# Kernel tuning notes

Hardware: AMD Instinct MI355X
Metric: run time of the kernel (lower is better)

## Reference

```python
import jax, jax.numpy as jnp
import numpy as np

B, T, V, E, H, C = 256, 512, 100000, 128, 256, 2


def setup_inputs() -> dict:
    key = jax.random.key(0)
    ks = jax.random.split(key, 14)
    lens = jax.random.randint(ks[0], (B,), 1, T + 1)          # valid lengths in [1, T]
    seqs = jax.random.randint(ks[1], (B, T), 1, V)            # tokens 1..V-1 (0 = pad)
    valid = jnp.arange(T)[None, :] < lens[:, None]
    seqs = jnp.where(valid, seqs, 0)                           # padding_idx = 0
    embed = jax.random.normal(ks[2], (V, E), dtype=jnp.float32) * 0.02
    embed = embed.at[0].set(0.0)                               # padding row zeroed (torch padding_idx)
    s = 1.0 / np.sqrt(H)
    u = lambda k, sh: jax.random.uniform(k, sh, minval=-s, maxval=s, dtype=jnp.float32)
    return {
        "seqs": seqs, "lens": lens, "embed": embed,
        "W_ih_f": u(ks[3], (3 * H, E)), "W_hh_f": u(ks[4], (3 * H, H)),
        "b_ih_f": u(ks[5], (3 * H,)),   "b_hh_f": u(ks[6], (3 * H,)),
        "W_ih_b": u(ks[7], (3 * H, E)), "W_hh_b": u(ks[8], (3 * H, H)),
        "b_ih_b": u(ks[9], (3 * H,)),   "b_hh_b": u(ks[10], (3 * H,)),
        "W_fc": u(ks[11], (C, 2 * H)),  "b_fc": u(ks[12], (C,)),
    }


def _gru_last_hidden(x, W_ih, W_hh, b_ih, b_hh, lens):
    """Run a single-direction GRU over x [B,T,E]; return hidden at step lens-1, [B,H].
    PyTorch GRU gate order: r, z, n."""
    xp = jnp.einsum('bte,ge->btg', x, W_ih) + b_ih             # [B,T,3H], one big GEMM up front

    def step(h, xp_t):                                          # xp_t: [B,3H]
        hp = h @ W_hh.T + b_hh
        r = jax.nn.sigmoid(xp_t[:, :H] + hp[:, :H])
        z = jax.nn.sigmoid(xp_t[:, H:2 * H] + hp[:, H:2 * H])
        n = jnp.tanh(xp_t[:, 2 * H:] + r * hp[:, 2 * H:])
        h_new = (1.0 - z) * n + z * h
        return h_new, h_new

    h0 = jnp.zeros((x.shape[0], H), dtype=x.dtype)
    _, hs = jax.lax.scan(step, h0, jnp.swapaxes(xp, 0, 1))     # hs: [T,B,H]
    return hs[lens - 1, jnp.arange(x.shape[0])]                # hidden at last valid step


def reference(seqs, lens, embed, W_ih_f, W_hh_f, b_ih_f, b_hh_f,
              W_ih_b, W_hh_b, b_ih_b, b_hh_b, W_fc, b_fc):
    x = embed[seqs]                                            # [B,T,E]
    # forward direction: final hidden at t = len-1 (packed-sequence semantics)
    h_f = _gru_last_hidden(x, W_ih_f, W_hh_f, b_ih_f, b_hh_f, lens)
    # backward direction: reverse each sequence within its valid length, then same scan
    idx = jnp.clip(lens[:, None] - 1 - jnp.arange(T)[None, :], 0, T - 1)  # [B,T]
    x_rev = jnp.take_along_axis(x, idx[:, :, None], axis=1)
    h_b = _gru_last_hidden(x_rev, W_ih_b, W_hh_b, b_ih_b, b_hh_b, lens)
    h = jnp.concatenate([h_f, h_b], axis=1)                    # [B,2H]
    return h @ W_fc.T + b_fc                                   # [B,C]
```

## Files before the change

kernel.cpp:

```cpp
#include <hip/hip_runtime.h>
#include <cstdint>
#include <cstddef>

#define B_   256
#define T_   512
#define E_   128
#define H_   256

typedef _Float16 f16x8 __attribute__((ext_vector_type(8)));
typedef _Float16 f16x4 __attribute__((ext_vector_type(4)));
typedef float    f32x4 __attribute__((ext_vector_type(4)));

__device__ __forceinline__ float sigm(float x) {
  return __builtin_amdgcn_rcpf(1.f + __expf(-x));
}
__device__ __forceinline__ float tanh_(float x) {
  float e = __expf(2.f * x);
  return 1.f - 2.f * __builtin_amdgcn_rcpf(1.f + e);
}
__device__ __forceinline__ void poll_ge(const int* p, int v) {
  while (__hip_atomic_load(p, __ATOMIC_ACQUIRE, __HIP_MEMORY_SCOPE_AGENT) < v)
    __builtin_amdgcn_s_sleep(4);
}

__global__ __launch_bounds__(256) void prep_kernel(
    const float* __restrict__ whhf, const float* __restrict__ whhb,
    const float* __restrict__ wihf, const float* __restrict__ wihb,
    _Float16* __restrict__ WSW,
    const int* __restrict__ lens, int* __restrict__ order, int* __restrict__ flags)
{
  if (blockIdx.x == 288) {
    int i = threadIdx.x;
    for (int k = i; k < 1024; k += 256) flags[k] = 0;
    for (int k = i; k < 512;  k += 256) flags[1024 + k] = -1;
    int li = lens[i];
    int rank = 0;
    for (int k = 0; k < B_; ++k) {
      int lk = lens[k];
      rank += (lk > li) || (lk == li && k < i);
    }
    order[rank] = i;
    return;
  }
  int idx = blockIdx.x * 256 + threadIdx.x;
  int lane = idx & 63;
  int tile = (idx >> 6) % 48;
  int kc   = (idx / 3072) % 12;
  int dir  = idx / 36864;
  int ncol = tile * 16 + (lane & 15);
  int quad = lane >> 4;
  const float* src;
  if (kc < 8) {
    const float* w = dir ? whhb : whhf;
    src = w + (size_t)ncol * H_ + kc * 32 + quad * 8;
  } else {
    const float* w = dir ? wihb : wihf;
    src = w + (size_t)ncol * E_ + (kc - 8) * 32 + quad * 8;
  }
  f16x8 v;
  #pragma unroll
  for (int j = 0; j < 8; ++j) v[j] = (_Float16)src[j];
  *(f16x8*)(WSW + (size_t)idx * 8) = v;
}

#define XPSLAB 196608
__global__ __launch_bounds__(512, 1) void fused_kernel(
    const _Float16* __restrict__ WSW, const int* __restrict__ seqs,
    const float* __restrict__ embed,
    const float* __restrict__ bihf, const float* __restrict__ bhhf,
    const float* __restrict__ bihb, const float* __restrict__ bhhb,
    const int* __restrict__ lens, const int* __restrict__ order,
    _Float16* __restrict__ XP, int* __restrict__ FLAGS, float* __restrict__ hcat)
{
  __shared__ __align__(16) char smem[147968];
  __shared__ int s_row[16], s_len[16];

  const int bid = blockIdx.x, tid = threadIdx.x;
  const int w = tid >> 6, lane = tid & 63, lm = lane & 15, lq = lane >> 4;

  if (bid < 32) {
    const int g = bid, dir = g & 1, grp = g >> 1;
    _Float16* wl = (_Float16*)smem;
    _Float16* hb = (_Float16*)(smem + 131072);
    if (tid < 16) { int r = order[grp * 16 + tid]; s_row[tid] = r; s_len[tid] = lens[r]; }
    for (int i = tid; i < 2 * 16 * 264; i += 512) hb[i] = (_Float16)0.f;

    const _Float16* wsd = WSW + (size_t)dir * 294912 + (size_t)lane * 8;
    #pragma unroll
    for (int kc = 0; kc < 8; ++kc) {
      *(f16x8*)(wl + ((w * 2 + 0) * 8 + kc) * 512 + lane * 8) =
          *(const f16x8*)(wsd + (size_t)kc * 24576 + (32 + 2 * w) * 512);
      *(f16x8*)(wl + ((w * 2 + 1) * 8 + kc) * 512 + lane * 8) =
          *(const f16x8*)(wsd + (size_t)kc * 24576 + (33 + 2 * w) * 512);
    }
    f16x8 wh[4][8];
    #pragma unroll
    for (int kc = 0; kc < 8; ++kc) {
      wh[0][kc] = *(const f16x8*)(wsd + (size_t)kc * 24576 + (2 * w)      * 512);
      wh[1][kc] = *(const f16x8*)(wsd + (size_t)kc * 24576 + (2 * w + 1)  * 512);
      wh[2][kc] = *(const f16x8*)(wsd + (size_t)kc * 24576 + (16 + 2 * w) * 512);
      wh[3][kc] = *(const f16x8*)(wsd + (size_t)kc * 24576 + (17 + 2 * w) * 512);
    }
    #pragma unroll
    for (int s = 0; s < 4; ++s)
      #pragma unroll
      for (int kc = 0; kc < 8; ++kc)
        asm volatile("" : "+a"(wh[s][kc]));
    const float* bhh = dir ? bhhb : bhhf;
    f16x4 bhn[2];
    #pragma unroll
    for (int th = 0; th < 2; ++th) {
      float4 b = *(const float4*)(bhh + 512 + 32 * w + th * 16 + lq * 4);
      bhn[th][0] = (_Float16)b.x; bhn[th][1] = (_Float16)b.y;
      bhn[th][2] = (_Float16)b.z; bhn[th][3] = (_Float16)b.w;
    }
    __syncthreads();
    const int len_l = s_len[lm];
    int ml = 1;
    #pragma unroll
    for (int i = 0; i < 16; ++i) ml = max(ml, s_len[i]);

    int* doneP  = FLAGS + 1024 + g * 16;
    const int* readyA = FLAGS + g * 32;
    const int* readyB = FLAGS + g * 32 + 16;
    float h32r[2][4] = {};

    for (int t = 0; t < ml; ++t) {
      if ((t & 15) == 0) {
        if (tid == 0) {
          if (t) __hip_atomic_store(doneP, (t >> 4) - 1,
                                    __ATOMIC_RELEASE, __HIP_MEMORY_SCOPE_AGENT);
          poll_ge(readyA, (t >> 4) + 1);
          poll_ge(readyB, (t >> 4) + 1);
        }
        __syncthreads();
      }
      const _Float16* sb = XP + ((size_t)((((t >> 4) & 1) * 32 + g)) * 16 + (t & 15)) * 12288
                           + lq * 64 + lm * 4;
      f16x4 xp[6];
      xp[0] = *(const f16x4*)(sb + (2 * w)      * 256);
      xp[1] = *(const f16x4*)(sb + (2 * w + 1)  * 256);
      xp[2] = *(const f16x4*)(sb + (16 + 2 * w) * 256);
      xp[3] = *(const f16x4*)(sb + (17 + 2 * w) * 256);
      xp[4] = *(const f16x4*)(sb + (32 + 2 * w) * 256);
      xp[5] = *(const f16x4*)(sb + (33 + 2 * w) * 256);

      f32x4 acc[6] = {};
      #pragma unroll
      for (int i = 0; i < 4; ++i) {
        acc[4][i] = (float)bhn[0][i];
        acc[5][i] = (float)bhn[1][i];
      }
      const _Float16* hrow = hb + ((size_t)(t & 1) * 16 + lm) * 264 + lq * 8;
      #pragma unroll
      for (int kc = 0; kc < 8; ++kc) {
        f16x8 hf = *(const f16x8*)(hrow + kc * 32);
        acc[0] = __builtin_amdgcn_mfma_f32_16x16x32_f16(wh[0][kc], hf, acc[0], 0, 0, 0);
        acc[1] = __builtin_amdgcn_mfma_f32_16x16x32_f16(wh[1][kc], hf, acc[1], 0, 0, 0);
        acc[2] = __builtin_amdgcn_mfma_f32_16x16x32_f16(wh[2][kc], hf, acc[2], 0, 0, 0);
        acc[3] = __builtin_amdgcn_mfma_f32_16x16x32_f16(wh[3][kc], hf, acc[3], 0, 0, 0);
        f16x8 w4 = *(const f16x8*)(wl + ((w * 2 + 0) * 8 + kc) * 512 + lane * 8);
        acc[4] = __builtin_amdgcn_mfma_f32_16x16x32_f16(w4, hf, acc[4], 0, 0, 0);
        f16x8 w5 = *(const f16x8*)(wl + ((w * 2 + 1) * 8 + kc) * 512 + lane * 8);
        acc[5] = __builtin_amdgcn_mfma_f32_16x16x32_f16(w5, hf, acc[5], 0, 0, 0);
      }
      #pragma unroll
      for (int th = 0; th < 2; ++th) {
        f16x4 pk;
        #pragma unroll
        for (int i = 0; i < 4; ++i) {
          float r = sigm((float)xp[th][i]     + acc[th][i]);
          float z = sigm((float)xp[2 + th][i] + acc[2 + th][i]);
          float n = tanh_((float)xp[4 + th][i] + r * acc[4 + th][i]);
          float hn = (t < len_l) ? (n + z * (h32r[th][i] - n)) : h32r[th][i];
          h32r[th][i] = hn;
          pk[i] = (_Float16)hn;
        }
        *(f16x4*)(hb + ((size_t)((t + 1) & 1) * 16 + lm) * 264 + 32 * w + th * 16 + lq * 4) = pk;
      }
      __syncthreads();
    }
    if (tid == 0)
      __hip_atomic_store(doneP, 999, __ATOMIC_RELEASE, __HIP_MEMORY_SCOPE_AGENT);
    {
      const int rowb = s_row[lm];
      #pragma unroll
      for (int th = 0; th < 2; ++th) {
        float4 o; o.x = h32r[th][0]; o.y = h32r[th][1]; o.z = h32r[th][2]; o.w = h32r[th][3];
        *(float4*)(&hcat[(size_t)rowb * (2 * H_) + dir * H_ + 32 * w + th * 16 + lq * 4]) = o;
      }
    }
  } else {
    const int k_ = bid - 32;
    const int g = (k_ & 7) + 8 * (k_ >> 4), half = (k_ >> 3) & 1;
    const int dir = g & 1, grp = g >> 1;
    _Float16* xs = (_Float16*)smem;
    if (tid < 16) { int r = order[grp * 16 + tid]; s_row[tid] = r; s_len[tid] = lens[r]; }
    __syncthreads();
    int ml = 1;
    #pragma unroll
    for (int i = 0; i < 16; ++i) ml = max(ml, s_len[i]);
    const int nch = (ml + 15) >> 4;

    const int chain = tid >> 5, q = tid & 31;
    const int rowb = s_row[chain], lenr = s_len[chain];
    const _Float16* wsd = WSW + (size_t)dir * 294912 + (size_t)lane * 8;
    const float* bih = dir ? bihb : bihf;
    const float* bhh = dir ? bhhb : bhhf;
    const int* doneP = FLAGS + 1024 + g * 16;
    int* readyP = FLAGS + g * 32 + half * 16;

    f16x8 wA[6][4];
    float bb[6][4];
    #pragma unroll
    for (int ti = 0; ti < 6; ++ti) {
      const int tile = w + 8 * ti;
      #pragma unroll
      for (int kc = 0; kc < 4; ++kc)
        wA[ti][kc] = *(const f16x8*)(wsd + (size_t)(8 + kc) * 24576 + tile * 512);
      float4 bias = *(const float4*)(bih + tile * 16 + lq * 4);
      if (tile < 32) {
        float4 b2 = *(const float4*)(bhh + tile * 16 + lq * 4);
        bias.x += b2.x; bias.y += b2.y; bias.z += b2.z; bias.w += b2.w;
      }
      bb[ti][0] = bias.x; bb[ti][1] = bias.y; bb[ti][2] = bias.z; bb[ti][3] = bias.w;
    }

    for (int c = 0; c < nch; ++c) {
      if (c >= 2) { if (tid == 0) poll_ge(doneP, c - 2); __syncthreads(); }
      _Float16* slab = XP + (size_t)((c & 1) * 32 + g) * XPSLAB;
      #pragma unroll
      for (int batch = 0; batch < 2; ++batch) {
        #pragma unroll
        for (int sb = 0; sb < 4; ++sb) {
          int s = c * 16 + half * 8 + batch * 4 + sb;
          int p = dir ? (lenr - 1 - s) : s;
          p = min(max(p, 0), T_ - 1);
          int tok = seqs[(size_t)rowb * T_ + p];
          float4 f = *(const float4*)(embed + (size_t)tok * E_ + q * 4);
          f16x4 h4; h4[0] = (_Float16)f.x; h4[1] = (_Float16)f.y;
          h4[2] = (_Float16)f.z; h4[3] = (_Float16)f.w;
          *(f16x4*)(xs + ((size_t)sb * 16 + chain) * 136 + q * 4) = h4;
        }
        __syncthreads();
        f16x8 bx[4][4];
        #pragma unroll
        for (int sb = 0; sb < 4; ++sb)
          #pragma unroll
          for (int kc = 0; kc < 4; ++kc)
            bx[sb][kc] = *(const f16x8*)(xs + ((size_t)sb * 16 + lm) * 136 + kc * 32 + lq * 8);
        #pragma unroll
        for (int ti = 0; ti < 6; ++ti) {
          const int tile = w + 8 * ti;
          f32x4 acc[4] = {};
          #pragma unroll
          for (int kc = 0; kc < 4; ++kc) {
            acc[0] = __builtin_amdgcn_mfma_f32_16x16x32_f16(wA[ti][kc], bx[0][kc], acc[0], 0, 0, 0);
            acc[1] = __builtin_amdgcn_mfma_f32_16x16x32_f16(wA[ti][kc], bx[1][kc], acc[1], 0, 0, 0);
            acc[2] = __builtin_amdgcn_mfma_f32_16x16x32_f16(wA[ti][kc], bx[2][kc], acc[2], 0, 0, 0);
            acc[3] = __builtin_amdgcn_mfma_f32_16x16x32_f16(wA[ti][kc], bx[3][kc], acc[3], 0, 0, 0);
          }
          #pragma unroll
          for (int sb = 0; sb < 4; ++sb) {
            int s_local = half * 8 + batch * 4 + sb;
            f16x4 o;
            #pragma unroll
            for (int i = 0; i < 4; ++i) o[i] = (_Float16)(acc[sb][i] + bb[ti][i]);
            *(f16x4*)(slab + (size_t)s_local * 12288 + tile * 256 + lq * 64 + lm * 4) = o;
          }
        }
        __syncthreads();
      }
      if (tid == 0)
        __hip_atomic_store(readyP, c + 1, __ATOMIC_RELEASE, __HIP_MEMORY_SCOPE_AGENT);
    }
  }
}

__global__ __launch_bounds__(512) void fc_kernel(
    const float* __restrict__ hcat, const float* __restrict__ wfc,
    const float* __restrict__ bfc, float* __restrict__ out)
{
  const int b = blockIdx.x, t = threadIdx.x;
  float h  = hcat[(size_t)b * 512 + t];
  float p0 = h * wfc[t];
  float p1 = h * wfc[512 + t];
  #pragma unroll
  for (int off = 32; off > 0; off >>= 1) {
    p0 += __shfl_down(p0, off);
    p1 += __shfl_down(p1, off);
  }
  __shared__ float s0[8], s1[8];
  if ((t & 63) == 0) { s0[t >> 6] = p0; s1[t >> 6] = p1; }
  __syncthreads();
  if (t == 0) {
    float a = bfc[0], c = bfc[1];
    #pragma unroll
    for (int i = 0; i < 8; ++i) { a += s0[i]; c += s1[i]; }
    out[b * 2 + 0] = a;
    out[b * 2 + 1] = c;
  }
}

extern "C" void kernel_launch(void* const* d_in, const int* in_sizes, int n_in,
                              void* d_out, int out_size, void* d_ws, size_t ws_size,
                              hipStream_t stream)
{
  (void)in_sizes; (void)n_in; (void)out_size; (void)ws_size;
  const int*   seqs  = (const int*)d_in[0];
  const int*   lens  = (const int*)d_in[1];
  const float* embed = (const float*)d_in[2];
  const float* wihf  = (const float*)d_in[3];
  const float* whhf  = (const float*)d_in[4];
  const float* bihf  = (const float*)d_in[5];
  const float* bhhf  = (const float*)d_in[6];
  const float* wihb  = (const float*)d_in[7];
  const float* whhb  = (const float*)d_in[8];
  const float* bihb  = (const float*)d_in[9];
  const float* bhhb  = (const float*)d_in[10];
  const float* wfc   = (const float*)d_in[11];
  const float* bfc   = (const float*)d_in[12];
  float* out = (float*)d_out;

  char* ws = (char*)d_ws;
  _Float16* WSW = (_Float16*)ws;
  size_t off = 1179648;
  _Float16* XP  = (_Float16*)(ws + off); off += (size_t)2 * 32 * XPSLAB * 2;
  float* HCAT   = (float*)(ws + off);    off += (size_t)B_ * 2 * H_ * 4;
  int* ORDER    = (int*)(ws + off);      off += 1024;
  int* FLAGS    = (int*)(ws + off);      off += 6144;

  prep_kernel<<<289, 256, 0, stream>>>(whhf, whhb, wihf, wihb, WSW, lens, ORDER, FLAGS);
  fused_kernel<<<96, 512, 0, stream>>>(WSW, seqs, embed, bihf, bhhf, bihb, bhhb,
                                       lens, ORDER, XP, FLAGS, HCAT);
  fc_kernel<<<B_, 512, 0, stream>>>(HCAT, wfc, bfc, out);
}
```

Measured before the change: 1.161 ms.

## Halve fused kernel block to 256 threads, doubling per-wave GRU gate tiles

```diff
diff --git a/kernel.cpp b/kernel.cpp
--- a/kernel.cpp
+++ b/kernel.cpp
@@ -64,7 +64,7 @@
 }
 
 #define XPSLAB 196608
-__global__ __launch_bounds__(512, 1) void fused_kernel(
+__global__ __launch_bounds__(256, 1) void fused_kernel(
     const _Float16* __restrict__ WSW, const int* __restrict__ seqs,
     const float* __restrict__ embed,
     const float* __restrict__ bihf, const float* __restrict__ bhhf,
@@ -83,34 +83,36 @@
     _Float16* wl = (_Float16*)smem;
     _Float16* hb = (_Float16*)(smem + 131072);
     if (tid < 16) { int r = order[grp * 16 + tid]; s_row[tid] = r; s_len[tid] = lens[r]; }
-    for (int i = tid; i < 2 * 16 * 264; i += 512) hb[i] = (_Float16)0.f;
+    for (int i = tid; i < 2 * 16 * 264; i += 256) hb[i] = (_Float16)0.f;
 
     const _Float16* wsd = WSW + (size_t)dir * 294912 + (size_t)lane * 8;
     #pragma unroll
-    for (int kc = 0; kc < 8; ++kc) {
-      *(f16x8*)(wl + ((w * 2 + 0) * 8 + kc) * 512 + lane * 8) =
-          *(const f16x8*)(wsd + (size_t)kc * 24576 + (32 + 2 * w) * 512);
-      *(f16x8*)(wl + ((w * 2 + 1) * 8 + kc) * 512 + lane * 8) =
-          *(const f16x8*)(wsd + (size_t)kc * 24576 + (33 + 2 * w) * 512);
-    }
-    f16x8 wh[4][8];
-    #pragma unroll
-    for (int kc = 0; kc < 8; ++kc) {
-      wh[0][kc] = *(const f16x8*)(wsd + (size_t)kc * 24576 + (2 * w)      * 512);
-      wh[1][kc] = *(const f16x8*)(wsd + (size_t)kc * 24576 + (2 * w + 1)  * 512);
-      wh[2][kc] = *(const f16x8*)(wsd + (size_t)kc * 24576 + (16 + 2 * w) * 512);
-      wh[3][kc] = *(const f16x8*)(wsd + (size_t)kc * 24576 + (17 + 2 * w) * 512);
-    }
-    #pragma unroll
-    for (int s = 0; s < 4; ++s)
+    for (int th = 0; th < 4; ++th)
       #pragma unroll
       for (int kc = 0; kc < 8; ++kc)
-        asm volatile("" : "+a"(wh[s][kc]));
+        *(f16x8*)(wl + (((w * 4 + th) * 8) + kc) * 512 + lane * 8) =
+            *(const f16x8*)(wsd + (size_t)kc * 24576 + (32 + 4 * w + th) * 512);
+
+    f16x8 whr[4][8], whz[4][8];
+    #pragma unroll
+    for (int th = 0; th < 4; ++th)
+      #pragma unroll
+      for (int kc = 0; kc < 8; ++kc) {
+        whr[th][kc] = *(const f16x8*)(wsd + (size_t)kc * 24576 + (4 * w + th)      * 512);
+        whz[th][kc] = *(const f16x8*)(wsd + (size_t)kc * 24576 + (16 + 4 * w + th) * 512);
+      }
+    #pragma unroll
+    for (int th = 0; th < 4; ++th)
+      #pragma unroll
+      for (int kc = 0; kc < 8; ++kc) {
+        asm volatile("" : "+a"(whr[th][kc]));
+        asm volatile("" : "+a"(whz[th][kc]));
+      }
     const float* bhh = dir ? bhhb : bhhf;
-    f16x4 bhn[2];
-    #pragma unroll
-    for (int th = 0; th < 2; ++th) {
-      float4 b = *(const float4*)(bhh + 512 + 32 * w + th * 16 + lq * 4);
+    f16x4 bhn[4];
+    #pragma unroll
+    for (int th = 0; th < 4; ++th) {
+      float4 b = *(const float4*)(bhh + 512 + 64 * w + th * 16 + lq * 4);
       bhn[th][0] = (_Float16)b.x; bhn[th][1] = (_Float16)b.y;
       bhn[th][2] = (_Float16)b.z; bhn[th][3] = (_Float16)b.w;
     }
@@ -123,7 +125,7 @@
     int* doneP  = FLAGS + 1024 + g * 16;
     const int* readyA = FLAGS + g * 32;
     const int* readyB = FLAGS + g * 32 + 16;
-    float h32r[2][4] = {};
+    float h32r[4][4] = {};
 
     for (int t = 0; t < ml; ++t) {
       if ((t & 15) == 0) {
@@ -137,46 +139,45 @@
       }
       const _Float16* sb = XP + ((size_t)((((t >> 4) & 1) * 32 + g)) * 16 + (t & 15)) * 12288
                            + lq * 64 + lm * 4;
-      f16x4 xp[6];
-      xp[0] = *(const f16x4*)(sb + (2 * w)      * 256);
-      xp[1] = *(const f16x4*)(sb + (2 * w + 1)  * 256);
-      xp[2] = *(const f16x4*)(sb + (16 + 2 * w) * 256);
-      xp[3] = *(const f16x4*)(sb + (17 + 2 * w) * 256);
-      xp[4] = *(const f16x4*)(sb + (32 + 2 * w) * 256);
-      xp[5] = *(const f16x4*)(sb + (33 + 2 * w) * 256);
-
-      f32x4 acc[6] = {};
-      #pragma unroll
-      for (int i = 0; i < 4; ++i) {
-        acc[4][i] = (float)bhn[0][i];
-        acc[5][i] = (float)bhn[1][i];
-      }
+      f16x4 xr[4], xz[4], xn[4];
+      #pragma unroll
+      for (int th = 0; th < 4; ++th) {
+        xr[th] = *(const f16x4*)(sb + (4 * w + th)      * 256);
+        xz[th] = *(const f16x4*)(sb + (16 + 4 * w + th) * 256);
+        xn[th] = *(const f16x4*)(sb + (32 + 4 * w + th) * 256);
+      }
+
+      f32x4 accr[4] = {}, accz[4] = {}, accn[4];
+      #pragma unroll
+      for (int th = 0; th < 4; ++th)
+        #pragma unroll
+        for (int i = 0; i < 4; ++i) accn[th][i] = (float)bhn[th][i];
+
       const _Float16* hrow = hb + ((size_t)(t & 1) * 16 + lm) * 264 + lq * 8;
       #pragma unroll
       for (int kc = 0; kc < 8; ++kc) {
         f16x8 hf = *(const f16x8*)(hrow + kc * 32);
-        acc[0] = __builtin_amdgcn_mfma_f32_16x16x32_f16(wh[0][kc], hf, acc[0], 0, 0, 0);
-        acc[1] = __builtin_amdgcn_mfma_f32_16x16x32_f16(wh[1][kc], hf, acc[1], 0, 0, 0);
-        acc[2] = __builtin_amdgcn_mfma_f32_16x16x32_f16(wh[2][kc], hf, acc[2], 0, 0, 0);
-        acc[3] = __builtin_amdgcn_mfma_f32_16x16x32_f16(wh[3][kc], hf, acc[3], 0, 0, 0);
-        f16x8 w4 = *(const f16x8*)(wl + ((w * 2 + 0) * 8 + kc) * 512 + lane * 8);
-        acc[4] = __builtin_amdgcn_mfma_f32_16x16x32_f16(w4, hf, acc[4], 0, 0, 0);
-        f16x8 w5 = *(const f16x8*)(wl + ((w * 2 + 1) * 8 + kc) * 512 + lane * 8);
-        acc[5] = __builtin_amdgcn_mfma_f32_16x16x32_f16(w5, hf, acc[5], 0, 0, 0);
-      }
-      #pragma unroll
-      for (int th = 0; th < 2; ++th) {
+        #pragma unroll
+        for (int th = 0; th < 4; ++th) {
+          f16x8 wn = *(const f16x8*)(wl + (((w * 4 + th) * 8) + kc) * 512 + lane * 8);
+          accr[th] = __builtin_amdgcn_mfma_f32_16x16x32_f16(whr[th][kc], hf, accr[th], 0, 0, 0);
+          accz[th] = __builtin_amdgcn_mfma_f32_16x16x32_f16(whz[th][kc], hf, accz[th], 0, 0, 0);
+          accn[th] = __builtin_amdgcn_mfma_f32_16x16x32_f16(wn,          hf, accn[th], 0, 0, 0);
+        }
+      }
+      #pragma unroll
+      for (int th = 0; th < 4; ++th) {
         f16x4 pk;
         #pragma unroll
         for (int i = 0; i < 4; ++i) {
-          float r = sigm((float)xp[th][i]     + acc[th][i]);
-          float z = sigm((float)xp[2 + th][i] + acc[2 + th][i]);
-          float n = tanh_((float)xp[4 + th][i] + r * acc[4 + th][i]);
+          float r = sigm((float)xr[th][i] + accr[th][i]);
+          float z = sigm((float)xz[th][i] + accz[th][i]);
+          float n = tanh_((float)xn[th][i] + r * accn[th][i]);
           float hn = (t < len_l) ? (n + z * (h32r[th][i] - n)) : h32r[th][i];
           h32r[th][i] = hn;
           pk[i] = (_Float16)hn;
         }
-        *(f16x4*)(hb + ((size_t)((t + 1) & 1) * 16 + lm) * 264 + 32 * w + th * 16 + lq * 4) = pk;
+        *(f16x4*)(hb + ((size_t)((t + 1) & 1) * 16 + lm) * 264 + 64 * w + th * 16 + lq * 4) = pk;
       }
       __syncthreads();
     }
@@ -185,9 +186,9 @@
     {
       const int rowb = s_row[lm];
       #pragma unroll
-      for (int th = 0; th < 2; ++th) {
+      for (int th = 0; th < 4; ++th) {
         float4 o; o.x = h32r[th][0]; o.y = h32r[th][1]; o.z = h32r[th][2]; o.w = h32r[th][3];
-        *(float4*)(&hcat[(size_t)rowb * (2 * H_) + dir * H_ + 32 * w + th * 16 + lq * 4]) = o;
+        *(float4*)(&hcat[(size_t)rowb * (2 * H_) + dir * H_ + 64 * w + th * 16 + lq * 4]) = o;
       }
     }
   } else {
@@ -202,7 +203,7 @@
     for (int i = 0; i < 16; ++i) ml = max(ml, s_len[i]);
     const int nch = (ml + 15) >> 4;
 
-    const int chain = tid >> 5, q = tid & 31;
+    const int chain = tid >> 4, q = tid & 15;
     const int rowb = s_row[chain], lenr = s_len[chain];
     const _Float16* wsd = WSW + (size_t)dir * 294912 + (size_t)lane * 8;
     const float* bih = dir ? bihb : bihf;
@@ -210,11 +211,11 @@
     const int* doneP = FLAGS + 1024 + g * 16;
     int* readyP = FLAGS + g * 32 + half * 16;
 
-    f16x8 wA[6][4];
-    float bb[6][4];
-    #pragma unroll
-    for (int ti = 0; ti < 6; ++ti) {
-      const int tile = w + 8 * ti;
+    f16x8 wA[12][4];
+    float bb[12][4];
+    #pragma unroll
+    for (int ti = 0; ti < 12; ++ti) {
+      const int tile = w + 4 * ti;
       #pragma unroll
       for (int kc = 0; kc < 4; ++kc)
         wA[ti][kc] = *(const f16x8*)(wsd + (size_t)(8 + kc) * 24576 + tile * 512);
@@ -237,10 +238,16 @@
           int p = dir ? (lenr - 1 - s) : s;
           p = min(max(p, 0), T_ - 1);
           int tok = seqs[(size_t)rowb * T_ + p];
-          float4 f = *(const float4*)(embed + (size_t)tok * E_ + q * 4);
-          f16x4 h4; h4[0] = (_Float16)f.x; h4[1] = (_Float16)f.y;
-          h4[2] = (_Float16)f.z; h4[3] = (_Float16)f.w;
-          *(f16x4*)(xs + ((size_t)sb * 16 + chain) * 136 + q * 4) = h4;
+          const float* er = embed + (size_t)tok * E_ + q * 8;
+          float4 f0 = *(const float4*)(er);
+          float4 f1 = *(const float4*)(er + 4);
+          f16x4 h0; h0[0] = (_Float16)f0.x; h0[1] = (_Float16)f0.y;
+          h0[2] = (_Float16)f0.z; h0[3] = (_Float16)f0.w;
+          f16x4 h1; h1[0] = (_Float16)f1.x; h1[1] = (_Float16)f1.y;
+          h1[2] = (_Float16)f1.z; h1[3] = (_Float16)f1.w;
+          _Float16* xd = xs + ((size_t)sb * 16 + chain) * 136 + q * 8;
+          *(f16x4*)(xd)     = h0;
+          *(f16x4*)(xd + 4) = h1;
         }
         __syncthreads();
         f16x8 bx[4][4];
@@ -250,8 +257,8 @@
           for (int kc = 0; kc < 4; ++kc)
             bx[sb][kc] = *(const f16x8*)(xs + ((size_t)sb * 16 + lm) * 136 + kc * 32 + lq * 8);
         #pragma unroll
-        for (int ti = 0; ti < 6; ++ti) {
-          const int tile = w + 8 * ti;
+        for (int ti = 0; ti < 12; ++ti) {
+          const int tile = w + 4 * ti;
           f32x4 acc[4] = {};
           #pragma unroll
           for (int kc = 0; kc < 4; ++kc) {
@@ -331,7 +338,7 @@
   int* FLAGS    = (int*)(ws + off);      off += 6144;
 
   prep_kernel<<<289, 256, 0, stream>>>(whhf, whhb, wihf, wihb, WSW, lens, ORDER, FLAGS);
-  fused_kernel<<<96, 512, 0, stream>>>(WSW, seqs, embed, bihf, bhhf, bihb, bhhb,
+  fused_kernel<<<96, 256, 0, stream>>>(WSW, seqs, embed, bihf, bhhf, bihb, bhhb,
                                        lens, ORDER, XP, FLAGS, HCAT);
   fc_kernel<<<B_, 512, 0, stream>>>(HCAT, wfc, bfc, out);
 }
```

After: 1.510 ms. 30.1% more time.

## Interleave two sequence groups per recurrent block to overlap MFMA and gate math

Applied to the files above, without the earlier changes.

```diff
diff --git a/kernel.cpp b/kernel.cpp
--- a/kernel.cpp
+++ b/kernel.cpp
@@ -73,17 +73,23 @@
     _Float16* __restrict__ XP, int* __restrict__ FLAGS, float* __restrict__ hcat)
 {
   __shared__ __align__(16) char smem[147968];
-  __shared__ int s_row[16], s_len[16];
+  __shared__ int s_row[32], s_len[32];
 
   const int bid = blockIdx.x, tid = threadIdx.x;
   const int w = tid >> 6, lane = tid & 63, lm = lane & 15, lq = lane >> 4;
 
-  if (bid < 32) {
-    const int g = bid, dir = g & 1, grp = g >> 1;
-    _Float16* wl = (_Float16*)smem;
-    _Float16* hb = (_Float16*)(smem + 131072);
-    if (tid < 16) { int r = order[grp * 16 + tid]; s_row[tid] = r; s_len[tid] = lens[r]; }
-    for (int i = tid; i < 2 * 16 * 264; i += 512) hb[i] = (_Float16)0.f;
+  if (bid < 16) {
+    const int gA = bid, gB = bid + 16, dir = bid & 1;
+    const int grpA = bid >> 1, grpB = (bid >> 1) + 8;
+    _Float16* wl  = (_Float16*)smem;
+    _Float16* hbA = (_Float16*)(smem + 131072);
+    _Float16* hbB = (_Float16*)(smem + 139520);
+    if (tid < 32) {
+      int which = tid >> 4, i = tid & 15;
+      int r = order[(which ? grpB : grpA) * 16 + i];
+      s_row[tid] = r; s_len[tid] = lens[r];
+    }
+    for (int i = tid; i < 2 * 16 * 264; i += 512) hbA[i] = (_Float16)0.f;
 
     const _Float16* wsd = WSW + (size_t)dir * 294912 + (size_t)lane * 8;
     #pragma unroll
@@ -97,15 +103,14 @@
     #pragma unroll
     for (int kc = 0; kc < 8; ++kc) {
       wh[0][kc] = *(const f16x8*)(wsd + (size_t)kc * 24576 + (2 * w)      * 512);
+      asm volatile("" : "+a"(wh[0][kc]));
       wh[1][kc] = *(const f16x8*)(wsd + (size_t)kc * 24576 + (2 * w + 1)  * 512);
+      asm volatile("" : "+a"(wh[1][kc]));
       wh[2][kc] = *(const f16x8*)(wsd + (size_t)kc * 24576 + (16 + 2 * w) * 512);
+      asm volatile("" : "+a"(wh[2][kc]));
       wh[3][kc] = *(const f16x8*)(wsd + (size_t)kc * 24576 + (17 + 2 * w) * 512);
-    }
-    #pragma unroll
-    for (int s = 0; s < 4; ++s)
-      #pragma unroll
-      for (int kc = 0; kc < 8; ++kc)
-        asm volatile("" : "+a"(wh[s][kc]));
+      asm volatile("" : "+a"(wh[3][kc]));
+    }
     const float* bhh = dir ? bhhb : bhhf;
     f16x4 bhn[2];
     #pragma unroll
@@ -115,83 +120,155 @@
       bhn[th][2] = (_Float16)b.z; bhn[th][3] = (_Float16)b.w;
     }
     __syncthreads();
-    const int len_l = s_len[lm];
-    int ml = 1;
-    #pragma unroll
-    for (int i = 0; i < 16; ++i) ml = max(ml, s_len[i]);
-
-    int* doneP  = FLAGS + 1024 + g * 16;
-    const int* readyA = FLAGS + g * 32;
-    const int* readyB = FLAGS + g * 32 + 16;
-    float h32r[2][4] = {};
-
-    for (int t = 0; t < ml; ++t) {
+    const int len_lA = s_len[lm], len_lB = s_len[16 + lm];
+    int mlA = 1, mlB = 1;
+    #pragma unroll
+    for (int i = 0; i < 16; ++i) { mlA = max(mlA, s_len[i]); mlB = max(mlB, s_len[16 + i]); }
+    const int nchB = (mlB + 15) >> 4;
+
+    int* donePA = FLAGS + 1024 + gA * 16;
+    int* donePB = FLAGS + 1024 + gB * 16;
+    const int* readyA0 = FLAGS + gA * 32;
+    const int* readyA1 = FLAGS + gA * 32 + 16;
+    const int* readyB0 = FLAGS + gB * 32;
+    const int* readyB1 = FLAGS + gB * 32 + 16;
+
+    f32x4 accA[6], accB[6];
+    f16x4 xpA[6], xpB[6];
+    float h32rA[2][4] = {}, h32rB[2][4] = {};
+
+    for (int t = 0; t < mlA; ++t) {
       if ((t & 15) == 0) {
+        int q = t >> 4;
         if (tid == 0) {
-          if (t) __hip_atomic_store(doneP, (t >> 4) - 1,
-                                    __ATOMIC_RELEASE, __HIP_MEMORY_SCOPE_AGENT);
-          poll_ge(readyA, (t >> 4) + 1);
-          poll_ge(readyB, (t >> 4) + 1);
+          if (t) {
+            __hip_atomic_store(donePA, q - 1, __ATOMIC_RELEASE, __HIP_MEMORY_SCOPE_AGENT);
+            __hip_atomic_store(donePB, q - 1, __ATOMIC_RELEASE, __HIP_MEMORY_SCOPE_AGENT);
+          }
+          poll_ge(readyA0, q + 1);
+          poll_ge(readyA1, q + 1);
+          if (q < nchB) { poll_ge(readyB0, q + 1); poll_ge(readyB1, q + 1); }
         }
         __syncthreads();
       }
-      const _Float16* sb = XP + ((size_t)((((t >> 4) & 1) * 32 + g)) * 16 + (t & 15)) * 12288
-                           + lq * 64 + lm * 4;
-      f16x4 xp[6];
-      xp[0] = *(const f16x4*)(sb + (2 * w)      * 256);
-      xp[1] = *(const f16x4*)(sb + (2 * w + 1)  * 256);
-      xp[2] = *(const f16x4*)(sb + (16 + 2 * w) * 256);
-      xp[3] = *(const f16x4*)(sb + (17 + 2 * w) * 256);
-      xp[4] = *(const f16x4*)(sb + (32 + 2 * w) * 256);
-      xp[5] = *(const f16x4*)(sb + (33 + 2 * w) * 256);
-
-      f32x4 acc[6] = {};
-      #pragma unroll
-      for (int i = 0; i < 4; ++i) {
-        acc[4][i] = (float)bhn[0][i];
-        acc[5][i] = (float)bhn[1][i];
-      }
-      const _Float16* hrow = hb + ((size_t)(t & 1) * 16 + lm) * 264 + lq * 8;
-      #pragma unroll
-      for (int kc = 0; kc < 8; ++kc) {
-        f16x8 hf = *(const f16x8*)(hrow + kc * 32);
-        acc[0] = __builtin_amdgcn_mfma_f32_16x16x32_f16(wh[0][kc], hf, acc[0], 0, 0, 0);
-        acc[1] = __builtin_amdgcn_mfma_f32_16x16x32_f16(wh[1][kc], hf, acc[1], 0, 0, 0);
-        acc[2] = __builtin_amdgcn_mfma_f32_16x16x32_f16(wh[2][kc], hf, acc[2], 0, 0, 0);
-        acc[3] = __builtin_amdgcn_mfma_f32_16x16x32_f16(wh[3][kc], hf, acc[3], 0, 0, 0);
-        f16x8 w4 = *(const f16x8*)(wl + ((w * 2 + 0) * 8 + kc) * 512 + lane * 8);
-        acc[4] = __builtin_amdgcn_mfma_f32_16x16x32_f16(w4, hf, acc[4], 0, 0, 0);
-        f16x8 w5 = *(const f16x8*)(wl + ((w * 2 + 1) * 8 + kc) * 512 + lane * 8);
-        acc[5] = __builtin_amdgcn_mfma_f32_16x16x32_f16(w5, hf, acc[5], 0, 0, 0);
-      }
+      {
+        const _Float16* sbA = XP + ((size_t)((((t >> 4) & 1) * 32 + gA)) * 16 + (t & 15))
+                              * 12288 + lq * 64 + lm * 4;
+        xpA[0] = *(const f16x4*)(sbA + (2 * w)      * 256);
+        xpA[1] = *(const f16x4*)(sbA + (2 * w + 1)  * 256);
+        xpA[2] = *(const f16x4*)(sbA + (16 + 2 * w) * 256);
+        xpA[3] = *(const f16x4*)(sbA + (17 + 2 * w) * 256);
+        xpA[4] = *(const f16x4*)(sbA + (32 + 2 * w) * 256);
+        xpA[5] = *(const f16x4*)(sbA + (33 + 2 * w) * 256);
+        #pragma unroll
+        for (int j = 0; j < 4; ++j) { accA[j][0]=0.f; accA[j][1]=0.f; accA[j][2]=0.f; accA[j][3]=0.f; }
+        #pragma unroll
+        for (int i = 0; i < 4; ++i) { accA[4][i] = (float)bhn[0][i]; accA[5][i] = (float)bhn[1][i]; }
+        const _Float16* hrow = hbA + (size_t)lm * 264 + lq * 8;
+        #pragma unroll
+        for (int kc = 0; kc < 8; ++kc) {
+          f16x8 hf = *(const f16x8*)(hrow + kc * 32);
+          f16x8 w4 = *(const f16x8*)(wl + ((w * 2 + 0) * 8 + kc) * 512 + lane * 8);
+          f16x8 w5 = *(const f16x8*)(wl + ((w * 2 + 1) * 8 + kc) * 512 + lane * 8);
+          accA[0] = __builtin_amdgcn_mfma_f32_16x16x32_f16(wh[0][kc], hf, accA[0], 0, 0, 0);
+          accA[1] = __builtin_amdgcn_mfma_f32_16x16x32_f16(wh[1][kc], hf, accA[1], 0, 0, 0);
+          accA[2] = __builtin_amdgcn_mfma_f32_16x16x32_f16(wh[2][kc], hf, accA[2], 0, 0, 0);
+          accA[3] = __builtin_amdgcn_mfma_f32_16x16x32_f16(wh[3][kc], hf, accA[3], 0, 0, 0);
+          accA[4] = __builtin_amdgcn_mfma_f32_16x16x32_f16(w4, hf, accA[4], 0, 0, 0);
+          accA[5] = __builtin_amdgcn_mfma_f32_16x16x32_f16(w5, hf, accA[5], 0, 0, 0);
+        }
+        if (t > 0) {
+          int tprev = t - 1;
+          #pragma unroll
+          for (int th = 0; th < 2; ++th) {
+            f16x4 pk;
+            #pragma unroll
+            for (int i = 0; i < 4; ++i) {
+              float r = sigm((float)xpB[th][i]     + accB[th][i]);
+              float z = sigm((float)xpB[2 + th][i] + accB[2 + th][i]);
+              float n = tanh_((float)xpB[4 + th][i] + r * accB[4 + th][i]);
+              float hn = (tprev < len_lB) ? (n + z * (h32rB[th][i] - n)) : h32rB[th][i];
+              h32rB[th][i] = hn;
+              pk[i] = (_Float16)hn;
+            }
+            *(f16x4*)(hbB + (size_t)lm * 264 + 32 * w + th * 16 + lq * 4) = pk;
+          }
+        }
+      }
+      __syncthreads();
+      {
+        const _Float16* sbB = XP + ((size_t)((((t >> 4) & 1) * 32 + gB)) * 16 + (t & 15))
+                              * 12288 + lq * 64 + lm * 4;
+        xpB[0] = *(const f16x4*)(sbB + (2 * w)      * 256);
+        xpB[1] = *(const f16x4*)(sbB + (2 * w + 1)  * 256);
+        xpB[2] = *(const f16x4*)(sbB + (16 + 2 * w) * 256);
+        xpB[3] = *(const f16x4*)(sbB + (17 + 2 * w) * 256);
+        xpB[4] = *(const f16x4*)(sbB + (32 + 2 * w) * 256);
+        xpB[5] = *(const f16x4*)(sbB + (33 + 2 * w) * 256);
+        #pragma unroll
+        for (int j = 0; j < 4; ++j) { accB[j][0]=0.f; accB[j][1]=0.f; accB[j][2]=0.f; accB[j][3]=0.f; }
+        #pragma unroll
+        for (int i = 0; i < 4; ++i) { accB[4][i] = (float)bhn[0][i]; accB[5][i] = (float)bhn[1][i]; }
+        const _Float16* hrow = hbB + (size_t)lm * 264 + lq * 8;
+        #pragma unroll
+        for (int kc = 0; kc < 8; ++kc) {
+          f16x8 hf = *(const f16x8*)(hrow + kc * 32);
+          f16x8 w4 = *(const f16x8*)(wl + ((w * 2 + 0) * 8 + kc) * 512 + lane * 8);
+          f16x8 w5 = *(const f16x8*)(wl + ((w * 2 + 1) * 8 + kc) * 512 + lane * 8);
+          accB[0] = __builtin_amdgcn_mfma_f32_16x16x32_f16(wh[0][kc], hf, accB[0], 0, 0, 0);
+          accB[1] = __builtin_amdgcn_mfma_f32_16x16x32_f16(wh[1][kc], hf, accB[1], 0, 0, 0);
+          accB[2] = __builtin_amdgcn_mfma_f32_16x16x32_f16(wh[2][kc], hf, accB[2], 0, 0, 0);
+          accB[3] = __builtin_amdgcn_mfma_f32_16x16x32_f16(wh[3][kc], hf, accB[3], 0, 0, 0);
+          accB[4] = __builtin_amdgcn_mfma_f32_16x16x32_f16(w4, hf, accB[4], 0, 0, 0);
+          accB[5] = __builtin_amdgcn_mfma_f32_16x16x32_f16(w5, hf, accB[5], 0, 0, 0);
+        }
+        #pragma unroll
+        for (int th = 0; th < 2; ++th) {
+          f16x4 pk;
+          #pragma unroll
+          for (int i = 0; i < 4; ++i) {
+            float r = sigm((float)xpA[th][i]     + accA[th][i]);
+            float z = sigm((float)xpA[2 + th][i] + accA[2 + th][i]);
+            float n = tanh_((float)xpA[4 + th][i] + r * accA[4 + th][i]);
+            float hn = (t < len_lA) ? (n + z * (h32rA[th][i] - n)) : h32rA[th][i];
+            h32rA[th][i] = hn;
+            pk[i] = (_Float16)hn;
+          }
+          *(f16x4*)(hbA + (size_t)lm * 264 + 32 * w + th * 16 + lq * 4) = pk;
+        }
+      }
+      __syncthreads();
+    }
+    {
+      int tprev = mlA - 1;
       #pragma unroll
       for (int th = 0; th < 2; ++th) {
-        f16x4 pk;
         #pragma unroll
         for (int i = 0; i < 4; ++i) {
-          float r = sigm((float)xp[th][i]     + acc[th][i]);
-          float z = sigm((float)xp[2 + th][i] + acc[2 + th][i]);
-          float n = tanh_((float)xp[4 + th][i] + r * acc[4 + th][i]);
-          float hn = (t < len_l) ? (n + z * (h32r[th][i] - n)) : h32r[th][i];
-          h32r[th][i] = hn;
-          pk[i] = (_Float16)hn;
-        }
-        *(f16x4*)(hb + ((size_t)((t + 1) & 1) * 16 + lm) * 264 + 32 * w + th * 16 + lq * 4) = pk;
-      }
-      __syncthreads();
-    }
-    if (tid == 0)
-      __hip_atomic_store(doneP, 999, __ATOMIC_RELEASE, __HIP_MEMORY_SCOPE_AGENT);
+          float r = sigm((float)xpB[th][i]     + accB[th][i]);
+          float z = sigm((float)xpB[2 + th][i] + accB[2 + th][i]);
+          float n = tanh_((float)xpB[4 + th][i] + r * accB[4 + th][i]);
+          float hn = (tprev < len_lB) ? (n + z * (h32rB[th][i] - n)) : h32rB[th][i];
+          h32rB[th][i] = hn;
+        }
+      }
+    }
+    if (tid == 0) {
+      __hip_atomic_store(donePA, 999, __ATOMIC_RELEASE, __HIP_MEMORY_SCOPE_AGENT);
+      __hip_atomic_store(donePB, 999, __ATOMIC_RELEASE, __HIP_MEMORY_SCOPE_AGENT);
+    }
     {
-      const int rowb = s_row[lm];
+      const int rowbA = s_row[lm], rowbB = s_row[16 + lm];
       #pragma unroll
       for (int th = 0; th < 2; ++th) {
-        float4 o; o.x = h32r[th][0]; o.y = h32r[th][1]; o.z = h32r[th][2]; o.w = h32r[th][3];
-        *(float4*)(&hcat[(size_t)rowb * (2 * H_) + dir * H_ + 32 * w + th * 16 + lq * 4]) = o;
+        float4 oa; oa.x = h32rA[th][0]; oa.y = h32rA[th][1]; oa.z = h32rA[th][2]; oa.w = h32rA[th][3];
+        *(float4*)(&hcat[(size_t)rowbA * (2 * H_) + dir * H_ + 32 * w + th * 16 + lq * 4]) = oa;
+        float4 ob; ob.x = h32rB[th][0]; ob.y = h32rB[th][1]; ob.z = h32rB[th][2]; ob.w = h32rB[th][3];
+        *(float4*)(&hcat[(size_t)rowbB * (2 * H_) + dir * H_ + 32 * w + th * 16 + lq * 4]) = ob;
       }
     }
   } else {
-    const int k_ = bid - 32;
+    const int k_ = bid - 16;
     const int g = (k_ & 7) + 8 * (k_ >> 4), half = (k_ >> 3) & 1;
     const int dir = g & 1, grp = g >> 1;
     _Float16* xs = (_Float16*)smem;
@@ -331,7 +408,7 @@
   int* FLAGS    = (int*)(ws + off);      off += 6144;
 
   prep_kernel<<<289, 256, 0, stream>>>(whhf, whhb, wihf, wihb, WSW, lens, ORDER, FLAGS);
-  fused_kernel<<<96, 512, 0, stream>>>(WSW, seqs, embed, bihf, bhhf, bihb, bhhb,
+  fused_kernel<<<80, 512, 0, stream>>>(WSW, seqs, embed, bihf, bhhf, bihb, bhhb,
                                        lens, ORDER, XP, FLAGS, HCAT);
   fc_kernel<<<B_, 512, 0, stream>>>(HCAT, wfc, bfc, out);
 }
```

Measured after the change: 2.399 ms. 107% more time.
